# Optimization experiments

Measured on AMD Instinct MI355X. Metric: run time of the kernel, lower is better.

Reference implementation:

```python
import jax, jax.numpy as jnp
import numpy as np
from jax import lax

BETA = 0.9
THRESHOLD = 0.75
SLOPE = 25.0  # snntorch fast_sigmoid default slope
EPS = 1e-5

@jax.custom_vjp
def spike_fn(x):
    # Heaviside forward, fast-sigmoid surrogate backward
    return (x > 0).astype(x.dtype)

def _spike_fwd(x):
    return spike_fn(x), x

def _spike_bwd(x, g):
    return (g / (SLOPE * jnp.abs(x) + 1.0) ** 2,)

spike_fn.defvjp(_spike_fwd, _spike_bwd)

def lif_preprocess(spikes, W, b):
    """SpikeSequencePreprocessor: 1x1 conv mix + per-timestep Leaky LIF (subtract reset).
    spikes: [B, C, T] -> [B, C, T] binary spike trace."""
    mixed = jnp.einsum('oc,bct->tbo', W, spikes) + b[None, None, :]  # [T,B,C]
    zero = jnp.zeros_like(mixed[0])

    def step(carry, x_t):
        mem, spk = carry
        # snntorch Leaky subtract-reset: reset uses previous step's spike
        mem = BETA * mem + x_t - spk * THRESHOLD
        spk = spike_fn(mem - THRESHOLD)
        return (mem, spk), spk

    _, trace = lax.scan(step, (zero, zero), mixed)  # [T,B,C]
    return jnp.transpose(trace, (1, 2, 0))  # [B,C,T]

def layer_norm(x):
    mu = jnp.mean(x, axis=-1, keepdims=True)
    var = jnp.var(x, axis=-1, keepdims=True)
    return (x - mu) / jnp.sqrt(var + EPS)

def setup_inputs() -> dict:
    key = jax.random.key(0)
    ks = jax.random.split(key, 16)
    B, C, T, H = 64, 256, 1024, 512
    transmit = (jax.random.uniform(ks[0], (B, C, T)) < 0.2).astype(jnp.float32)
    receive = (jax.random.uniform(ks[1], (B, 2, C, T)) < 0.2).astype(jnp.float32)
    eye = jnp.eye(C, dtype=jnp.float32)
    return {
        'transmit_spikes': transmit,
        'receive_spikes': receive,
        'base_distance': jax.random.normal(ks[2], (B, H), jnp.float32),
        'base_azimuth': jax.random.normal(ks[3], (B, H), jnp.float32),
        'base_elevation': jax.random.normal(ks[4], (B, H), jnp.float32),
        'W_tx': eye + 0.01 * jax.random.normal(ks[5], (C, C), jnp.float32),
        'b_tx': jnp.zeros((C,), jnp.float32),
        'W_rx': eye + 0.01 * jax.random.normal(ks[6], (C, C), jnp.float32),
        'b_rx': jnp.zeros((C,), jnp.float32),
        'Wd': jax.random.normal(ks[7], (H, C), jnp.float32) / np.sqrt(C),
        'bd': jnp.zeros((H,), jnp.float32),
        'Wa': jax.random.normal(ks[8], (H, C), jnp.float32) / np.sqrt(C),
        'ba': jnp.zeros((H,), jnp.float32),
        'We': jax.random.normal(ks[9], (H, C), jnp.float32) / np.sqrt(C),
        'be': jnp.zeros((H,), jnp.float32),
        'gain_d': jnp.float32(-1.2),
        'gain_a': jnp.float32(-1.2),
        'gain_e': jnp.float32(-1.2),
    }

def reference(transmit_spikes, receive_spikes, base_distance, base_azimuth,
              base_elevation, W_tx, b_tx, W_rx, b_rx, Wd, bd, Wa, ba, We, be,
              gain_d, gain_a, gain_e):
    B, _, C, T = receive_spikes.shape
    tx = lif_preprocess(transmit_spikes, W_tx, b_tx)                 # [B,C,T]
    rx = lif_preprocess(receive_spikes.reshape(B * 2, C, T), W_rx, b_rx)
    rx = rx.reshape(B, 2, C, T)                                      # [B,2,C,T]
    left, right = rx[:, 0], rx[:, 1]

    # pathway features (stand-in for build_pathway_features): per-channel time reductions
    f_dist = jnp.mean(tx, axis=-1)            # [B,C]
    f_azi = jnp.mean(left - right, axis=-1)   # [B,C]
    f_ele = jnp.mean(left + right, axis=-1)   # [B,C]
    spike_proxy = jnp.sum(rx, axis=-1)        # [B,2,C]

    rd = layer_norm(f_dist) @ Wd.T + bd
    ra = layer_norm(f_azi) @ Wa.T + ba
    re = layer_norm(f_ele) @ We.T + be

    sd = 0.3 * jax.nn.sigmoid(gain_d)
    sa = 0.3 * jax.nn.sigmoid(gain_a)
    se = 0.3 * jax.nn.sigmoid(gain_e)

    distance_latent = jax.nn.relu(base_distance + sd * rd)
    azimuth_latent = jax.nn.relu(base_azimuth + sa * ra)
    elevation_latent = jax.nn.relu(base_elevation + se * re)
    return distance_latent, azimuth_latent, elevation_latent, rx, spike_proxy
```

## Files before the change

kernel.cpp:

```cpp
#include <hip/hip_runtime.h>

#define B_   64
#define C_   256
#define T_   1024
#define H_   512
#define G_   192

#define OUT_DIST 0
#define OUT_AZI  (64*512)
#define OUT_ELE  (2*64*512)
#define OUT_RX   (3*64*512)
#define OUT_SP   (3*64*512 + 64*2*256*1024)

typedef _Float16 half8  __attribute__((ext_vector_type(8)));
typedef _Float16 half4v __attribute__((ext_vector_type(4)));
typedef float    floatx4 __attribute__((ext_vector_type(4)));

__global__ __launch_bounds__(256) void split_w(
    const float* __restrict__ Wtx, const float* __restrict__ Wrx,
    _Float16* __restrict__ w16)
{
    int e = blockIdx.x * 256 + threadIdx.x;
    int m = e >> 16;
    int i = e & 65535;
    float v = m ? Wrx[i] : Wtx[i];
    _Float16 hi = (_Float16)v;
    _Float16 lo = (_Float16)(v - (float)hi);
    w16[(size_t)m * 131072 + i] = hi;
    w16[(size_t)m * 131072 + 65536 + i] = lo;
}

__global__ __launch_bounds__(256, 3) void lif_mfma_v2(
    const float* __restrict__ transmit, const float* __restrict__ receive,
    const float* __restrict__ btx, const float* __restrict__ brx,
    const _Float16* __restrict__ w16, float* __restrict__ out,
    float* __restrict__ txCnt)
{
    __shared__ __align__(16) float ldsraw[8704];
    float*     Mlds = ldsraw;
    _Float16*  S16  = (_Float16*)ldsraw;

    const int tid = threadIdx.x;
    const int ot  = blockIdx.x / G_;
    const int g   = blockIdx.x % G_;
    const int o0  = ot * 64;
    const bool isRx = (g >= 64);
    const int gr  = g - 64;

    const float* Sg = isRx ? (receive + (size_t)gr * C_ * T_)
                           : (transmit + (size_t)g * C_ * T_);
    const _Float16* whi = w16 + (isRx ? 131072 : 0);
    const _Float16* wlo = whi + 65536;
    const float* bp = isRx ? brx : btx;

    const int lane = tid & 63;
    const int wv   = tid >> 6;
    const int col  = lane & 15;
    const int quad = lane >> 4;

    const int oA = o0 + wv * 16 + col;
    half8 Ahi[8], Alo[8];
#pragma unroll
    for (int ck = 0; ck < 8; ++ck) {
        Ahi[ck] = *(const half8*)(whi + (size_t)oA * 256 + ck * 32 + quad * 8);
        Alo[ck] = *(const half8*)(wlo + (size_t)oA * 256 + ck * 32 + quad * 8);
    }
    floatx4 bias4 = *(const floatx4*)(bp + o0 + wv * 16 + quad * 4);

    const int cq = tid & 31;
    const int tq = tid >> 5;

    float mem = 0.f, spk = 0.f, cnt = 0.f;

    for (int tt = 0; tt < 8; ++tt) {
        const int t0 = tt * 128;

        floatx4 acc[8];
#pragma unroll
        for (int nt = 0; nt < 8; ++nt) acc[nt] = bias4;

#pragma unroll
        for (int half = 0; half < 2; ++half) {
            const float* sb = Sg + (size_t)(half * 128 + cq * 4) * T_ + t0 + tq * 16;
#pragma unroll
            for (int p = 0; p < 2; ++p) {
                floatx4 v[4][2];
#pragma unroll
                for (int i = 0; i < 4; ++i)
#pragma unroll
                    for (int j4 = 0; j4 < 2; ++j4)
                        v[i][j4] = *(const floatx4*)(sb + (size_t)i * T_ + p * 8 + j4 * 4);
#pragma unroll
                for (int jj = 0; jj < 8; ++jj) {
                    int j4 = jj >> 2, r = jj & 3;
                    half4v h = { (_Float16)v[0][j4][r], (_Float16)v[1][j4][r],
                                 (_Float16)v[2][j4][r], (_Float16)v[3][j4][r] };
                    *(half4v*)(S16 + (size_t)(tq * 16 + p * 8 + jj) * 136 + cq * 4) = h;
                }
            }
            __syncthreads();

#pragma unroll
            for (int ckl = 0; ckl < 4; ++ckl) {
                const int ck = half * 4 + ckl;
#pragma unroll
                for (int nt = 0; nt < 8; ++nt) {
                    half8 bf = *(const half8*)(S16 + (size_t)(nt * 16 + col) * 136
                                               + ckl * 32 + quad * 8);
                    acc[nt] = __builtin_amdgcn_mfma_f32_16x16x32_f16(
                        Ahi[ck], bf, acc[nt], 0, 0, 0);
                    acc[nt] = __builtin_amdgcn_mfma_f32_16x16x32_f16(
                        Alo[ck], bf, acc[nt], 0, 0, 0);
                }
            }
            __syncthreads();
        }

#pragma unroll
        for (int nt = 0; nt < 8; ++nt) {
            int t = nt * 16 + col;
            *(floatx4*)(Mlds + (size_t)t * 68 + wv * 16 + quad * 4) = acc[nt];
        }
        __syncthreads();

        if (tid < 64) {
            if (isRx) {
#pragma unroll 8
                for (int t = 0; t < 128; ++t) {
                    float x = Mlds[t * 68 + tid];
                    mem = 0.9f * mem + x - spk * 0.75f;
                    spk = (mem > 0.75f) ? 1.0f : 0.0f;
                    cnt += spk;
                    Mlds[t * 68 + tid] = spk;
                }
            } else {
#pragma unroll 8
                for (int t = 0; t < 128; ++t) {
                    float x = Mlds[t * 68 + tid];
                    mem = 0.9f * mem + x - spk * 0.75f;
                    spk = (mem > 0.75f) ? 1.0f : 0.0f;
                    cnt += spk;
                }
            }
        }
        __syncthreads();

        if (isRx) {
            float* dstb = out + (size_t)OUT_RX + (size_t)gr * C_ * T_
                          + (size_t)o0 * T_ + t0;
            const int m = tid & 7;
            const int or0 = tid >> 3;
#pragma unroll
            for (int p = 0; p < 2; ++p) {
                int orow = or0 + p * 32;
                float* drow = dstb + (size_t)orow * T_;
#pragma unroll
                for (int q = 0; q < 4; ++q) {
                    int tq2 = m * 4 + q * 32;
                    float4 v = make_float4(Mlds[(tq2 + 0) * 68 + orow],
                                           Mlds[(tq2 + 1) * 68 + orow],
                                           Mlds[(tq2 + 2) * 68 + orow],
                                           Mlds[(tq2 + 3) * 68 + orow]);
                    *(float4*)(drow + tq2) = v;
                }
            }
        }
        __syncthreads();
    }

    if (tid < 64) {
        if (isRx) out[(size_t)OUT_SP + (size_t)gr * 256 + o0 + tid] = cnt;
        else      txCnt[(size_t)g * 256 + o0 + tid] = cnt;
    }
}

__global__ __launch_bounds__(128) void lif_gemm_scan(
    const float* __restrict__ transmit, const float* __restrict__ receive,
    const float* __restrict__ Wtx, const float* __restrict__ btx,
    const float* __restrict__ Wrx, const float* __restrict__ brx,
    float* __restrict__ out, float* __restrict__ wsF)
{
    __shared__ float lds[128 * 68];
    float* Slds = lds;
    float* Wlds = lds + 4096;
    float* Mlds = lds;

    const int tid = threadIdx.x;
    const int bx  = blockIdx.x;
    const int ot  = bx / G_;
    const int g   = bx % G_;
    const int o0  = ot * 64;
    const bool isRx = (g >= 64);

    const float* Sg = isRx ? (receive + (size_t)(g - 64) * C_ * T_)
                           : (transmit + (size_t)g * C_ * T_);
    const float* Wp = isRx ? Wrx : Wtx;
    const float* bp = isRx ? brx : btx;

    const int ti = tid & 15;
    const int oi = tid >> 4;
    const int tb = ti * 4;
    const int ob = oi * 4;

    float bias[2][4];
#pragma unroll
    for (int os = 0; os < 2; ++os)
#pragma unroll
        for (int j = 0; j < 4; ++j)
            bias[os][j] = bp[o0 + os * 32 + ob + j];

    float mem = 0.f, spk = 0.f, cnt = 0.f;

    for (int tt = 0; tt < 8; ++tt) {
        const int t0 = tt * 128;
        float acc[8][8];
#pragma unroll
        for (int ii = 0; ii < 8; ++ii)
#pragma unroll
            for (int jj = 0; jj < 8; ++jj)
                acc[ii][jj] = bias[jj >> 2][jj & 3];

        for (int kk = 0; kk < 8; ++kk) {
            const int c0 = kk * 32;
#pragma unroll
            for (int p = 0; p < 8; ++p) {
                int idx = tid + p * 128;
                int c = idx >> 5, t4 = idx & 31;
                *(float4*)(Slds + c * 128 + t4 * 4) =
                    *(const float4*)(Sg + (size_t)(c0 + c) * T_ + t0 + t4 * 4);
            }
#pragma unroll
            for (int p = 0; p < 4; ++p) {
                int idx = tid + p * 128;
                int o = idx >> 3, c4 = idx & 7;
                float4 w = *(const float4*)(Wp + (size_t)(o0 + o) * C_ + c0 + c4 * 4);
                Wlds[(c4 * 4 + 0) * 64 + o] = w.x;
                Wlds[(c4 * 4 + 1) * 64 + o] = w.y;
                Wlds[(c4 * 4 + 2) * 64 + o] = w.z;
                Wlds[(c4 * 4 + 3) * 64 + o] = w.w;
            }
            __syncthreads();
#pragma unroll 8
            for (int k = 0; k < 32; ++k) {
                float4 a0 = *(const float4*)(Slds + k * 128 + tb);
                float4 a1 = *(const float4*)(Slds + k * 128 + 64 + tb);
                float4 b0 = *(const float4*)(Wlds + k * 64 + ob);
                float4 b1 = *(const float4*)(Wlds + k * 64 + 32 + ob);
                float a[8]  = {a0.x, a0.y, a0.z, a0.w, a1.x, a1.y, a1.z, a1.w};
                float bv[8] = {b0.x, b0.y, b0.z, b0.w, b1.x, b1.y, b1.z, b1.w};
#pragma unroll
                for (int ii = 0; ii < 8; ++ii)
#pragma unroll
                    for (int jj = 0; jj < 8; ++jj)
                        acc[ii][jj] += a[ii] * bv[jj];
            }
            __syncthreads();
        }

#pragma unroll
        for (int ii = 0; ii < 8; ++ii) {
            int t = (ii >> 2) * 64 + tb + (ii & 3);
#pragma unroll
            for (int os = 0; os < 2; ++os) {
                float4 v = make_float4(acc[ii][os * 4 + 0], acc[ii][os * 4 + 1],
                                       acc[ii][os * 4 + 2], acc[ii][os * 4 + 3]);
                *(float4*)(Mlds + t * 68 + os * 32 + ob) = v;
            }
        }
        __syncthreads();

        if (tid < 64) {
#pragma unroll 4
            for (int t = 0; t < 128; ++t) {
                float x = Mlds[t * 68 + tid];
                mem = 0.9f * mem + x - spk * 0.75f;
                spk = (mem > 0.75f) ? 1.0f : 0.0f;
                cnt += spk;
                Mlds[t * 68 + tid] = spk;
            }
        }
        __syncthreads();

        if (isRx) {
            float* dst = out + (size_t)OUT_RX + (size_t)(g - 64) * C_ * T_
                         + (size_t)o0 * T_ + t0;
            int m = tid & 7;
            int orow0 = tid >> 3;
#pragma unroll
            for (int p = 0; p < 4; ++p) {
                int orow = orow0 + p * 16;
#pragma unroll
                for (int q = 0; q < 4; ++q) {
                    int tq = m * 4 + q * 32;
                    float4 v = make_float4(Mlds[(tq + 0) * 68 + orow],
                                           Mlds[(tq + 1) * 68 + orow],
                                           Mlds[(tq + 2) * 68 + orow],
                                           Mlds[(tq + 3) * 68 + orow]);
                    *(float4*)(dst + (size_t)orow * T_ + tq) = v;
                }
            }
        }
        __syncthreads();
    }

    if (tid < 64) {
        if (isRx) out[(size_t)OUT_SP + (size_t)(g - 64) * C_ + o0 + tid] = cnt;
        else      wsF[(size_t)g * C_ + o0 + tid] = cnt;
    }
}

__global__ __launch_bounds__(256) void heads_kernel(
    const float* __restrict__ wsF, const float* __restrict__ sp,
    const float* __restrict__ Wd, const float* __restrict__ bd,
    const float* __restrict__ Wa, const float* __restrict__ ba,
    const float* __restrict__ We, const float* __restrict__ be,
    const float* __restrict__ gd, const float* __restrict__ ga, const float* __restrict__ ge,
    const float* __restrict__ based, const float* __restrict__ basea, const float* __restrict__ basee,
    float* __restrict__ out)
{
    __shared__ float fv[256];
    __shared__ float red[8];
    const int tid = threadIdx.x;
    const int hd  = blockIdx.x >> 6;
    const int b   = blockIdx.x & 63;

    float f;
    if (hd == 0) {
        f = wsF[b * 256 + tid] * (1.f / 1024.f);
    } else {
        float l = sp[(2 * b) * 256 + tid];
        float r = sp[(2 * b + 1) * 256 + tid];
        f = ((hd == 1) ? (l - r) : (l + r)) * (1.f / 1024.f);
    }

    float v = f;
#pragma unroll
    for (int off = 32; off > 0; off >>= 1) v += __shfl_down(v, off, 64);
    if ((tid & 63) == 0) red[tid >> 6] = v;
    __syncthreads();
    float mu = (red[0] + red[1] + red[2] + red[3]) * (1.f / 256.f);

    float d = f - mu;
    v = d * d;
#pragma unroll
    for (int off = 32; off > 0; off >>= 1) v += __shfl_down(v, off, 64);
    if ((tid & 63) == 0) red[4 + (tid >> 6)] = v;
    __syncthreads();
    float var  = (red[4] + red[5] + red[6] + red[7]) * (1.f / 256.f);
    float rstd = rsqrtf(var + 1e-5f);
    fv[tid] = d * rstd;
    __syncthreads();

    const float* W    = (hd == 0) ? Wd : (hd == 1) ? Wa : We;
    const float* bb   = (hd == 0) ? bd : (hd == 1) ? ba : be;
    const float* base = (hd == 0) ? based : (hd == 1) ? basea : basee;
    float gain = (hd == 0) ? gd[0] : (hd == 1) ? ga[0] : ge[0];
    float s = 0.3f / (1.f + expf(-gain));

    const float4* fv4 = (const float4*)fv;
#pragma unroll
    for (int hh = 0; hh < 2; ++hh) {
        int h = tid + hh * 256;
        const float4* W4 = (const float4*)(W + (size_t)h * 256);
        float acc = 0.f;
#pragma unroll 8
        for (int c = 0; c < 64; ++c) {
            float4 w = W4[c];
            float4 x = fv4[c];
            acc += w.x * x.x + w.y * x.y + w.z * x.z + w.w * x.w;
        }
        float r = acc + bb[h];
        float o = base[b * 512 + h] + s * r;
        out[(size_t)hd * (64 * 512) + b * 512 + h] = fmaxf(o, 0.f);
    }
}

extern "C" void kernel_launch(void* const* d_in, const int* in_sizes, int n_in,
                              void* d_out, int out_size, void* d_ws, size_t ws_size,
                              hipStream_t stream)
{
    const float* transmit = (const float*)d_in[0];
    const float* receive  = (const float*)d_in[1];
    const float* based    = (const float*)d_in[2];
    const float* basea    = (const float*)d_in[3];
    const float* basee    = (const float*)d_in[4];
    const float* Wtx      = (const float*)d_in[5];
    const float* btx      = (const float*)d_in[6];
    const float* Wrx      = (const float*)d_in[7];
    const float* brx      = (const float*)d_in[8];
    const float* Wd       = (const float*)d_in[9];
    const float* bd       = (const float*)d_in[10];
    const float* Wa       = (const float*)d_in[11];
    const float* ba       = (const float*)d_in[12];
    const float* We       = (const float*)d_in[13];
    const float* be       = (const float*)d_in[14];
    const float* gd       = (const float*)d_in[15];
    const float* ga       = (const float*)d_in[16];
    const float* ge       = (const float*)d_in[17];
    float* out = (float*)d_out;
    float* spOut = out + (size_t)OUT_SP;

    const size_t need = 512 * 1024 + 64 * 1024;

    if (ws_size >= need) {
        _Float16* w16   = (_Float16*)d_ws;
        float*    txCnt = (float*)d_ws + 131072;

        hipLaunchKernelGGL(split_w, dim3(512), dim3(256), 0, stream,
                           Wtx, Wrx, w16);
        hipLaunchKernelGGL(lif_mfma_v2, dim3(768), dim3(256), 0, stream,
                           transmit, receive, btx, brx, w16, out, txCnt);
        hipLaunchKernelGGL(heads_kernel, dim3(192), dim3(256), 0, stream,
                           txCnt, spOut, Wd, bd, Wa, ba, We, be,
                           gd, ga, ge, based, basea, basee, out);
    } else {
        float* wsF = (float*)d_ws;
        hipLaunchKernelGGL(lif_gemm_scan, dim3(768), dim3(128), 0, stream,
                           transmit, receive, Wtx, btx, Wrx, brx, out, wsF);
        hipLaunchKernelGGL(heads_kernel, dim3(192), dim3(256), 0, stream,
                           wsF, spOut, Wd, bd, Wa, ba, We, be,
                           gd, ga, ge, based, basea, basee, out);
    }
}
```

Before: 415.1 us.

## Double-buffer spike tiles in LDS and split LIF scan across four waves

Reworks the MFMA LIF kernel so the input spike tiles are staged in 64-channel chunks into two ping-pong LDS buffers. The global loads for the next chunk are issued before the current chunk's MFMAs, which overlaps memory latency with matrix math and drops one barrier per chunk. The sequential LIF scan now runs on 16 lanes in each of the four waves instead of on a single wave, and is done in two 64-step halves so the epilogue buffer fits in the second LDS buffer. The cost is more barriers in the epilogue and shorter, less efficient output rows of 64 time steps.

```diff
diff --git a/kernel.cpp b/kernel.cpp
--- a/kernel.cpp
+++ b/kernel.cpp
@@ -13,7 +13,6 @@
 #define OUT_SP   (3*64*512 + 64*2*256*1024)
 
 typedef _Float16 half8  __attribute__((ext_vector_type(8)));
-typedef _Float16 half4v __attribute__((ext_vector_type(4)));
 typedef float    floatx4 __attribute__((ext_vector_type(4)));
 
 __global__ __launch_bounds__(256) void split_w(
@@ -30,15 +29,16 @@
     w16[(size_t)m * 131072 + 65536 + i] = lo;
 }
 
-__global__ __launch_bounds__(256, 3) void lif_mfma_v2(
+__global__ __launch_bounds__(256, 3) void lif_mfma_v4(
     const float* __restrict__ transmit, const float* __restrict__ receive,
     const float* __restrict__ btx, const float* __restrict__ brx,
     const _Float16* __restrict__ w16, float* __restrict__ out,
     float* __restrict__ txCnt)
 {
-    __shared__ __align__(16) float ldsraw[8704];
-    float*     Mlds = ldsraw;
-    _Float16*  S16  = (_Float16*)ldsraw;
+    __shared__ __align__(16) _Float16 s16[2 * 9216];
+    _Float16* bufA = s16;
+    _Float16* bufB = s16 + 9216;
+    float*    E    = (float*)bufB;
 
     const int tid = threadIdx.x;
     const int ot  = blockIdx.x / G_;
@@ -67,110 +67,134 @@
     }
     floatx4 bias4 = *(const floatx4*)(bp + o0 + wv * 16 + quad * 4);
 
-    const int cq = tid & 31;
-    const int tq = tid >> 5;
+    const int tq = tid & 31;
+    const int cq = tid >> 5;
 
     float mem = 0.f, spk = 0.f, cnt = 0.f;
 
+    {
+        const float* sb = Sg + (size_t)(cq * 8) * T_ + tq * 4;
+        floatx4 va[8];
+#pragma unroll
+        for (int i = 0; i < 8; ++i)
+            va[i] = *(const floatx4*)(sb + (size_t)i * T_);
+#pragma unroll
+        for (int j = 0; j < 4; ++j) {
+            half8 hv = { (_Float16)va[0][j], (_Float16)va[1][j],
+                         (_Float16)va[2][j], (_Float16)va[3][j],
+                         (_Float16)va[4][j], (_Float16)va[5][j],
+                         (_Float16)va[6][j], (_Float16)va[7][j] };
+            *(half8*)(bufA + (size_t)(tq * 4 + j) * 72 + cq * 8) = hv;
+        }
+        __syncthreads();
+    }
+
     for (int tt = 0; tt < 8; ++tt) {
-        const int t0 = tt * 128;
-
         floatx4 acc[8];
 #pragma unroll
         for (int nt = 0; nt < 8; ++nt) acc[nt] = bias4;
 
 #pragma unroll
-        for (int half = 0; half < 2; ++half) {
-            const float* sb = Sg + (size_t)(half * 128 + cq * 4) * T_ + t0 + tq * 16;
-#pragma unroll
-            for (int p = 0; p < 2; ++p) {
-                floatx4 v[4][2];
-#pragma unroll
-                for (int i = 0; i < 4; ++i)
-#pragma unroll
-                    for (int j4 = 0; j4 < 2; ++j4)
-                        v[i][j4] = *(const floatx4*)(sb + (size_t)i * T_ + p * 8 + j4 * 4);
-#pragma unroll
-                for (int jj = 0; jj < 8; ++jj) {
-                    int j4 = jj >> 2, r = jj & 3;
-                    half4v h = { (_Float16)v[0][j4][r], (_Float16)v[1][j4][r],
-                                 (_Float16)v[2][j4][r], (_Float16)v[3][j4][r] };
-                    *(half4v*)(S16 + (size_t)(tq * 16 + p * 8 + jj) * 136 + cq * 4) = h;
-                }
-            }
-            __syncthreads();
-
-#pragma unroll
-            for (int ckl = 0; ckl < 4; ++ckl) {
-                const int ck = half * 4 + ckl;
+        for (int qt = 0; qt < 4; ++qt) {
+            const _Float16* src = (qt & 1) ? bufB : bufA;
+            _Float16*       dst = (qt & 1) ? bufA : bufB;
+
+            const bool have = !(tt == 7 && qt == 3);
+            const int nqt = (qt + 1) & 3;
+            const int ntt = tt + (qt == 3 ? 1 : 0);
+
+            floatx4 va[8];
+            if (have) {
+                const float* sb = Sg + (size_t)(nqt * 64 + cq * 8) * T_
+                                  + ntt * 128 + tq * 4;
+#pragma unroll
+                for (int i = 0; i < 8; ++i)
+                    va[i] = *(const floatx4*)(sb + (size_t)i * T_);
+            }
+
+#pragma unroll
+            for (int ck2 = 0; ck2 < 2; ++ck2) {
+                const int ck = qt * 2 + ck2;
 #pragma unroll
                 for (int nt = 0; nt < 8; ++nt) {
-                    half8 bf = *(const half8*)(S16 + (size_t)(nt * 16 + col) * 136
-                                               + ckl * 32 + quad * 8);
+                    half8 bf = *(const half8*)(src + (size_t)(nt * 16 + col) * 72
+                                               + ck2 * 32 + quad * 8);
                     acc[nt] = __builtin_amdgcn_mfma_f32_16x16x32_f16(
                         Ahi[ck], bf, acc[nt], 0, 0, 0);
                     acc[nt] = __builtin_amdgcn_mfma_f32_16x16x32_f16(
                         Alo[ck], bf, acc[nt], 0, 0, 0);
                 }
             }
-            __syncthreads();
-        }
-
-#pragma unroll
-        for (int nt = 0; nt < 8; ++nt) {
-            int t = nt * 16 + col;
-            *(floatx4*)(Mlds + (size_t)t * 68 + wv * 16 + quad * 4) = acc[nt];
-        }
-        __syncthreads();
-
-        if (tid < 64) {
+
+            if (have) {
+#pragma unroll
+                for (int j = 0; j < 4; ++j) {
+                    half8 hv = { (_Float16)va[0][j], (_Float16)va[1][j],
+                                 (_Float16)va[2][j], (_Float16)va[3][j],
+                                 (_Float16)va[4][j], (_Float16)va[5][j],
+                                 (_Float16)va[6][j], (_Float16)va[7][j] };
+                    *(half8*)(dst + (size_t)(tq * 4 + j) * 72 + cq * 8) = hv;
+                }
+            }
+            __syncthreads();
+        }
+
+#pragma unroll
+        for (int h = 0; h < 2; ++h) {
+#pragma unroll
+            for (int ntl = 0; ntl < 4; ++ntl) {
+                int tl = ntl * 16 + col;
+                *(floatx4*)(E + (size_t)tl * 68 + wv * 16 + quad * 4) =
+                    acc[h * 4 + ntl];
+            }
+            __syncthreads();
+
+            if ((tid & 63) < 16) {
+                const int oloc = wv * 16 + (tid & 15);
+                if (isRx) {
+#pragma unroll 8
+                    for (int t = 0; t < 64; ++t) {
+                        float x = E[t * 68 + oloc];
+                        mem = 0.9f * mem + x - spk * 0.75f;
+                        spk = (mem > 0.75f) ? 1.0f : 0.0f;
+                        cnt += spk;
+                        E[t * 68 + oloc] = spk;
+                    }
+                } else {
+#pragma unroll 8
+                    for (int t = 0; t < 64; ++t) {
+                        float x = E[t * 68 + oloc];
+                        mem = 0.9f * mem + x - spk * 0.75f;
+                        spk = (mem > 0.75f) ? 1.0f : 0.0f;
+                        cnt += spk;
+                    }
+                }
+            }
+            __syncthreads();
+
             if (isRx) {
-#pragma unroll 8
-                for (int t = 0; t < 128; ++t) {
-                    float x = Mlds[t * 68 + tid];
-                    mem = 0.9f * mem + x - spk * 0.75f;
-                    spk = (mem > 0.75f) ? 1.0f : 0.0f;
-                    cnt += spk;
-                    Mlds[t * 68 + tid] = spk;
+                const int olane = tid >> 2;
+                const int tl4   = (tid & 3) * 4;
+                float* drow = out + (size_t)OUT_RX + (size_t)gr * C_ * T_
+                              + (size_t)(o0 + olane) * T_ + tt * 128 + h * 64;
+#pragma unroll
+                for (int q = 0; q < 4; ++q) {
+                    int t = tl4 + q * 16;
+                    float4 v = make_float4(E[(t + 0) * 68 + olane],
+                                           E[(t + 1) * 68 + olane],
+                                           E[(t + 2) * 68 + olane],
+                                           E[(t + 3) * 68 + olane]);
+                    *(float4*)(drow + t) = v;
                 }
-            } else {
-#pragma unroll 8
-                for (int t = 0; t < 128; ++t) {
-                    float x = Mlds[t * 68 + tid];
-                    mem = 0.9f * mem + x - spk * 0.75f;
-                    spk = (mem > 0.75f) ? 1.0f : 0.0f;
-                    cnt += spk;
-                }
-            }
-        }
-        __syncthreads();
-
-        if (isRx) {
-            float* dstb = out + (size_t)OUT_RX + (size_t)gr * C_ * T_
-                          + (size_t)o0 * T_ + t0;
-            const int m = tid & 7;
-            const int or0 = tid >> 3;
-#pragma unroll
-            for (int p = 0; p < 2; ++p) {
-                int orow = or0 + p * 32;
-                float* drow = dstb + (size_t)orow * T_;
-#pragma unroll
-                for (int q = 0; q < 4; ++q) {
-                    int tq2 = m * 4 + q * 32;
-                    float4 v = make_float4(Mlds[(tq2 + 0) * 68 + orow],
-                                           Mlds[(tq2 + 1) * 68 + orow],
-                                           Mlds[(tq2 + 2) * 68 + orow],
-                                           Mlds[(tq2 + 3) * 68 + orow]);
-                    *(float4*)(drow + tq2) = v;
-                }
-            }
-        }
-        __syncthreads();
-    }
-
-    if (tid < 64) {
-        if (isRx) out[(size_t)OUT_SP + (size_t)gr * 256 + o0 + tid] = cnt;
-        else      txCnt[(size_t)g * 256 + o0 + tid] = cnt;
+            }
+            __syncthreads();
+        }
+    }
+
+    if ((tid & 63) < 16) {
+        const int og = o0 + wv * 16 + (tid & 15);
+        if (isRx) out[(size_t)OUT_SP + (size_t)gr * 256 + og] = cnt;
+        else      txCnt[(size_t)g * 256 + og] = cnt;
     }
 }
 
@@ -408,7 +432,7 @@
 
         hipLaunchKernelGGL(split_w, dim3(512), dim3(256), 0, stream,
                            Wtx, Wrx, w16);
-        hipLaunchKernelGGL(lif_mfma_v2, dim3(768), dim3(256), 0, stream,
+        hipLaunchKernelGGL(lif_mfma_v4, dim3(768), dim3(256), 0, stream,
                            transmit, receive, btx, brx, w16, out, txCnt);
         hipLaunchKernelGGL(heads_kernel, dim3(192), dim3(256), 0, stream,
                            txCnt, spOut, Wd, bd, Wa, ba, We, be,
```

Result: faster. 379.2 us (-8.6%).
